# Kernel optimization log

Measured on AMD Instinct MI355X. Metric: run time of the kernel, lower is better.

## Reference

```python
import jax, jax.numpy as jnp
import numpy as np

B, C, H, W = 64, 256, 40, 40
NC = 12          # num_classes
WS = 5           # window_size
WHN, WWN = H // WS, W // WS  # 8, 8


def _window_coords():
    # Reproduces the torch __init__ construction of self.window_coords: [1, 8, 8, 2, 5, 5]
    bh = np.arange(WS) * 2.0 / (H - 1); bh = bh - bh.mean()
    bw = np.arange(WS) * 2.0 / (W - 1); bw = bw - bw.mean()
    ebh = np.tile(bh, WHN)  # [H]
    ebw = np.tile(bw, WWN)  # [W]
    # after meshgrid(ebw, ebh, ij) + permute(0,2,1): ch0 varies along cols (x), ch1 along rows (y)
    wc_x = np.broadcast_to(ebw[None, :], (H, W))
    wc_y = np.broadcast_to(ebh[:, None], (H, W))
    wc = np.stack([wc_x, wc_y], 0).reshape(2, WHN, WS, WWN, WS).transpose(1, 3, 0, 2, 4)
    return jnp.asarray(wc[None], dtype=jnp.float32)  # [1, WHN, WWN, 2, WS, WS]


def _bn(x, g, b, rm, rv):
    # eval-mode BatchNorm2d; x: [B, C, H, W], params per-channel
    inv = g / jnp.sqrt(rv + 1e-5)
    return x * inv[:, None, None] + (b - rm * inv)[:, None, None]


def _grid_sample(im, grid):
    # bilinear, padding_mode='zeros', align_corners=True; im [B,C,H,W], grid [B,H,W,2] (x,y)
    Bn, Cn, Hn, Wn = im.shape
    x = (grid[..., 0] + 1.0) * 0.5 * (Wn - 1)
    y = (grid[..., 1] + 1.0) * 0.5 * (Hn - 1)
    x0 = jnp.floor(x); x1 = x0 + 1.0
    y0 = jnp.floor(y); y1 = y0 + 1.0

    def corner(xi, yi, wgt):
        valid = (xi >= 0) & (xi <= Wn - 1) & (yi >= 0) & (yi <= Hn - 1)
        xc = jnp.clip(xi, 0, Wn - 1).astype(jnp.int32)
        yc = jnp.clip(yi, 0, Hn - 1).astype(jnp.int32)
        v = jax.vmap(lambda imb, yb, xb: imb[:, yb, xb])(im, yc, xc)  # [B,C,H,W]
        return v * (wgt * valid.astype(im.dtype))[:, None]

    return (corner(x0, y0, (x1 - x) * (y1 - y))
            + corner(x1, y0, (x - x0) * (y1 - y))
            + corner(x0, y1, (x1 - x) * (y - y0))
            + corner(x1, y1, (x - x0) * (y - y0)))


def setup_inputs() -> dict:
    key = jax.random.key(0)
    ks = jax.random.split(key, 16)
    f32 = jnp.float32
    return {
        "feats": jax.random.normal(ks[0], (B, C, H, W), f32),
        # distribution_head: Conv1x1 C->4*NC, BN, ReLU, grouped Conv1x1 4*NC->NC (groups=NC)
        "w1": jax.random.normal(ks[1], (NC * 4, C), f32) * 0.05,
        "b1": jax.random.normal(ks[2], (NC * 4,), f32) * 0.05,
        "g1": 1.0 + 0.1 * jax.random.normal(ks[3], (NC * 4,), f32),
        "be1": 0.1 * jax.random.normal(ks[4], (NC * 4,), f32),
        "rm1": 0.1 * jax.random.normal(ks[5], (NC * 4,), f32),
        "rv1": jax.random.uniform(ks[6], (NC * 4,), f32, 0.5, 1.5),
        "w2": jax.random.normal(ks[7], (NC, 4), f32) * 0.1,
        "b2": jax.random.normal(ks[8], (NC,), f32) * 0.05,
        # deformation_head: AvgPool5, BN(C), ReLU, Conv1x1 C->8
        "gd": 1.0 + 0.1 * jax.random.normal(ks[9], (C,), f32),
        "bed": 0.1 * jax.random.normal(ks[10], (C,), f32),
        "rmd": 0.1 * jax.random.normal(ks[11], (C,), f32),
        "rvd": jax.random.uniform(ks[12], (C,), f32, 0.5, 1.5),
        "wd": jax.random.normal(ks[13], (8, C), f32) * 0.05,
        "bd": jax.random.normal(ks[14], (8,), f32) * 0.05,
    }


def reference(feats, w1, b1, g1, be1, rm1, rv1, w2, b2, gd, bed, rmd, rvd, wd, bd):
    # ---- distribution_head ----
    x = jnp.einsum('bchw,oc->bohw', feats, w1) + b1[:, None, None]
    x = jax.nn.relu(_bn(x, g1, be1, rm1, rv1))
    x = x.reshape(B, NC, 4, H, W)  # grouped 1x1 conv, groups=NC
    y = jnp.einsum('bgchw,gc->bghw', x, w2) + b2[:, None, None]  # [B, NC, H, W]

    # ---- point_distribution (first batch element, as in original) ----
    hm = 1.0 - jnp.max(jax.nn.sigmoid(y[0]), axis=0)          # [H, W]
    hm = hm * (255.0 / jnp.max(hm))
    pointmap = (hm > (9.0 / 11.0) * 255.0).astype(feats.dtype)
    _ = pointmap  # due to the original's ==255 bug, pointmap never influences the mask

    # ---- point_mask: density map is always all-zero -> constant box (0,0,w=30,h=40) ----
    w_stride = W // 4  # 10
    mask_col = (jnp.arange(W) < 3 * w_stride).astype(feats.dtype)  # cols [0,30)
    fm = feats * mask_col + (1.0 - mask_col) * 1e-5
    f2 = fm + feats  # residual add from forward()

    # ---- region_deformer ----
    pooled = f2.reshape(B, C, WHN, WS, WWN, WS).mean(axis=(3, 5))  # AvgPool2d(5,5) -> [B,C,8,8]
    pooled = jax.nn.relu(_bn(pooled, gd, bed, rmd, rvd))
    co = jnp.einsum('bchw,oc->bhwo', pooled, wd) + bd              # [B,8,8,8]

    xr, yr, sx, sy = co[..., 0], co[..., 1], co[..., 2], co[..., 3]
    s = sx * sy
    tx = co[..., 4:6][..., None]  # [B,8,8,2,1]
    ty = co[..., 6:8][..., None]

    def rot(a):  # [[cos, sin], [-sin, cos]]
        return jnp.stack([jnp.cos(a), jnp.sin(a), -jnp.sin(a), jnp.cos(a)], -1).reshape(a.shape + (2, 2))

    M0 = (rot(xr) @ rot(yr)) * s[..., None, None]                  # Rx @ Ry @ (s*I)
    M1 = sx[..., None, None] * (rot(xr) @ ty) + tx                 # Rx @ (sx*I) @ ty + tx
    row3 = jnp.broadcast_to(jnp.array([0.0, 0.0, 1.0], feats.dtype), (B, WHN, WWN, 1, 3))
    M = jnp.concatenate([jnp.concatenate([M0, M1], -1), row3], -2)  # [B,8,8,3,3]

    wc = _window_coords().reshape(1, WHN, WWN, 2, WS * WS)
    wcp = jnp.concatenate([wc, jnp.ones((1, WHN, WWN, 1, WS * WS), feats.dtype)], -2)
    twc = M @ wcp                                                   # [B,8,8,3,25]
    den = twc[..., 2:3, :]
    den = jnp.where(den == 0.0, 1e-6, den)
    tw = twc[..., :2, :] / den
    coords = tw.reshape(B, WHN, WWN, 2, WS, WS).transpose(0, 3, 1, 4, 2, 5)  # [B,2,8,5,8,5]
    grid = coords.transpose(0, 2, 3, 4, 5, 1).reshape(B, H, W, 2)

    return _grid_sample(f2, grid)
```

## Files before the change

kernel.cpp:

```cpp
#include <hip/hip_runtime.h>
#include <math.h>

#define NB   64
#define NC_  256
#define NH   40
#define NW   40
#define NHW  1600
#define NWIN 64
#define CH   4
#define PW   44
#define IMS  1852

typedef float f32x4 __attribute__((ext_vector_type(4)));

__global__ __launch_bounds__(256) void pool_co_kernel(
    const float* __restrict__ feats,
    const float* __restrict__ gd, const float* __restrict__ bed,
    const float* __restrict__ rmd, const float* __restrict__ rvd,
    const float* __restrict__ wd, const float* __restrict__ bd,
    float4* __restrict__ cw4, int2* __restrict__ cbc)
{
    __shared__ float pl[8][NC_];
    __shared__ __align__(16) float swd[8 * NC_];
    __shared__ float sco[8][8];
    __shared__ float sM6[8][6];

    const int blk = blockIdx.x;
    const int b   = blk >> 3;
    const int wh  = blk & 7;
    const int t   = threadIdx.x;

    for (int i = t; i < 512; i += 256)
        ((f32x4*)swd)[i] = ((const f32x4*)wd)[i];

    {
        const f32x4* src = (const f32x4*)(feats + ((size_t)(b * NC_ + t)) * NHW
                                          + wh * 5 * NW);
        float acc[8] = {0.f, 0.f, 0.f, 0.f, 0.f, 0.f, 0.f, 0.f};
        #pragma unroll
        for (int r = 0; r < 5; ++r) {
            #pragma unroll
            for (int j = 0; j < 10; ++j) {
                const f32x4 v = src[r * 10 + j];
                #pragma unroll
                for (int k = 0; k < 4; ++k)
                    acc[(4 * j + k) / 5] += v[k];
            }
        }
        const float inv  = gd[t] / sqrtf(rvd[t] + 1e-5f);
        const float beta = bed[t] - rmd[t] * inv;
        #pragma unroll
        for (int ww = 0; ww < 8; ++ww) {
            const float mean = acc[ww] * (1.0f / 25.0f);
            const float f2m  = (ww < 6) ? (2.0f * mean) : (mean + 1e-5f);
            pl[ww][t] = fmaxf(f2m * inv + beta, 0.0f);
        }
    }
    __syncthreads();

    {
        const int w = t >> 5;
        const int s = t & 31;
        float po[8] = {0.f, 0.f, 0.f, 0.f, 0.f, 0.f, 0.f, 0.f};
        #pragma unroll
        for (int k = 0; k < 8; ++k) {
            const int c2 = s + 32 * k;
            const float p = pl[w][c2];
            #pragma unroll
            for (int o = 0; o < 8; ++o)
                po[o] += p * swd[o * NC_ + c2];
        }
        #pragma unroll
        for (int o = 0; o < 8; ++o) {
            #pragma unroll
            for (int off = 16; off > 0; off >>= 1)
                po[o] += __shfl_down(po[o], off, 32);
        }
        if (s == 0) {
            #pragma unroll
            for (int o = 0; o < 8; ++o) sco[w][o] = po[o] + bd[o];
        }
    }
    __syncthreads();

    if (t < 8) {
        const float xr = sco[t][0], yr = sco[t][1], sx = sco[t][2], sy = sco[t][3];
        const float tx0 = sco[t][4], tx1 = sco[t][5], ty0 = sco[t][6], ty1 = sco[t][7];
        const float cx = cosf(xr), sxr = sinf(xr);
        const float cy = cosf(yr), syr = sinf(yr);
        const float s = sx * sy;
        sM6[t][0] = (cx * cy - sxr * syr) * s;
        sM6[t][1] = (cx * syr + sxr * cy) * s;
        sM6[t][2] = sx * (cx * ty0 + sxr * ty1) + tx0;
        sM6[t][3] = (-sxr * cy - cx * syr) * s;
        sM6[t][4] = (-sxr * syr + cx * cy) * s;
        sM6[t][5] = sx * (-sxr * ty0 + cx * ty1) + tx1;
    }
    __syncthreads();

    if (t < 200) {
        const int w   = t / 25;
        const int pxi = t - w * 25;
        const int ii  = pxi / 5;
        const int jj  = pxi - ii * 5;
        const float* m = sM6[w];

        const float wcx = (float)(jj - 2) * (2.0f / 39.0f);
        const float wcy = (float)(ii - 2) * (2.0f / 39.0f);
        const float gx = m[0] * wcx + m[1] * wcy + m[2];
        const float gy = m[3] * wcx + m[4] * wcy + m[5];

        float x = (gx + 1.0f) * 19.5f;
        float y = (gy + 1.0f) * 19.5f;
        x = fminf(fmaxf(x, -1.0e6f), 1.0e6f);
        y = fminf(fmaxf(y, -1.0e6f), 1.0e6f);

        const float x0f = floorf(x), y0f = floorf(y);
        const int x0 = (int)x0f, y0 = (int)y0f;
        const int x1 = x0 + 1,  y1 = y0 + 1;
        const float fx = x - x0f, fy = y - y0f;

        const bool xv0 = (x0 >= 0) & (x0 <= NW - 1);
        const bool xv1 = (x1 >= 0) & (x1 <= NW - 1);
        const bool yv0 = (y0 >= 0) & (y0 <= NH - 1);
        const bool yv1 = (y1 >= 0) & (y1 <= NH - 1);

        const float w00 = (1.f - fx) * (1.f - fy) * (float)(xv0 && yv0);
        const float w01 = fx * (1.f - fy) * (float)(xv1 && yv0);
        const float w10 = (1.f - fx) * fy * (float)(xv0 && yv1);
        const float w11 = fx * fy * (float)(xv1 && yv1);

        const int xc0 = min(max(x0, 0), NW - 1);
        const int xc1 = min(max(x1, 0), NW - 1);
        const float a0 = (xc0 < 30) ? 2.f : 1.f;
        const float a1 = (xc1 < 30) ? 2.f : 1.f;
        const float d0 = (xc0 < 30) ? 0.f : 1e-5f;
        const float d1 = (xc1 < 30) ? 0.f : 1e-5f;

        float4 wvec;
        wvec.x = w00 * a0;
        wvec.y = w01 * a1;
        wvec.z = w10 * a0;
        wvec.w = w11 * a1;
        const float cst = (w00 + w10) * d0 + (w01 + w11) * d1;

        const int xb = min(max(x0, -1), NW - 1);
        const int yb = min(max(y0, -1), NH - 1);
        const int base = (yb + 1) * PW + xb;

        const int h    = wh * 5 + ii;
        const int wcol = w * 5 + jj;
        const int pidx = b * NHW + h * NW + wcol;
        cw4[pidx] = wvec;
        cbc[pidx] = make_int2(base, __float_as_int(cst));
    }
}

__global__ __launch_bounds__(320) void sample_lean_kernel(
    const float* __restrict__ feats,
    const float4* __restrict__ cw4, const int2* __restrict__ cbc,
    float* __restrict__ out)
{
    __shared__ __align__(16) float img[CH * IMS];

    const int blk = blockIdx.x;
    const int b   = blk >> 6;
    const int cg  = blk & 63;
    const int c0  = cg * CH;

    const float4* cwb = cw4 + (size_t)b * NHW;
    const int2*   cbb = cbc + (size_t)b * NHW;
    float4 wv[5];
    int2   pc[5];
    #pragma unroll
    for (int k = 0; k < 5; ++k) {
        wv[k] = cwb[k * 320 + threadIdx.x];
        pc[k] = cbb[k * 320 + threadIdx.x];
    }

    for (int i = threadIdx.x; i < CH * 63; i += 320) {
        const int cc = i / 63;
        const int t  = i - cc * 63;
        float* im = img + cc * IMS + 4;
        f32x4 z = {0.f, 0.f, 0.f, 0.f};
        if (t == 0)       *(f32x4*)(img + cc * IMS) = z;
        else if (t <= 11) *(f32x4*)(im + (t - 1) * 4) = z;
        else if (t <= 22) *(f32x4*)(im + 41 * PW + (t - 12) * 4) = z;
        else              *(f32x4*)(im + (t - 22) * PW + 40) = z;
    }

    {
        const int g   = threadIdx.x / 80;
        const int r80 = threadIdx.x - g * 80;
        const int rb  = r80 / 10;
        const int cb  = r80 - rb * 10;
        const float* src = feats + (size_t)(b * NC_ + c0 + g) * NHW;
        float* dst = img + g * IMS + 4 + PW;
        #pragma unroll
        for (int m = 0; m < 5; ++m) {
            const f32x4 v = *((const f32x4*)src + (m * 80 + r80));
            *(f32x4*)(dst + (m * 8 + rb) * PW + cb * 4) = v;
        }
    }
    __syncthreads();

    float* dstb = out + (size_t)(b * NC_ + c0) * NHW;

    #pragma unroll
    for (int k = 0; k < 5; ++k) {
        const int px = k * 320 + threadIdx.x;
        const int   base = pc[k].x;
        const float cst  = __int_as_float(pc[k].y);
        #pragma unroll
        for (int cc = 0; cc < CH; ++cc) {
            const float* ip = img + cc * IMS + 4 + base;
            const float r = cst + wv[k].x * ip[0]  + wv[k].y * ip[1]
                                + wv[k].z * ip[PW] + wv[k].w * ip[PW + 1];
            __builtin_nontemporal_store(r, &dstb[(size_t)cc * NHW + px]);
        }
    }
}

__global__ __launch_bounds__(256) void pool_bn_kernel(
    const float* __restrict__ feats,
    const float* __restrict__ gd, const float* __restrict__ bed,
    const float* __restrict__ rmd, const float* __restrict__ rvd,
    float* __restrict__ pooled)
{
    __shared__ __align__(16) float img[NHW];
    const int bc = blockIdx.x;
    const int b  = bc >> 8;
    const int c  = bc & 255;

    const float4* src4 = (const float4*)(feats + (size_t)bc * NHW);
    for (int i = threadIdx.x; i < NHW / 4; i += 256)
        ((float4*)img)[i] = src4[i];
    __syncthreads();

    if (threadIdx.x < NWIN) {
        const int win = threadIdx.x;
        const int wh  = win >> 3;
        const int ww  = win & 7;
        const int base = (wh * 5) * NW + ww * 5;
        float sum = 0.f;
        #pragma unroll
        for (int i = 0; i < 5; ++i)
            #pragma unroll
            for (int j = 0; j < 5; ++j)
                sum += img[base + i * NW + j];
        float mean = sum * (1.0f / 25.0f);
        float f2m  = (ww < 6) ? (2.0f * mean) : (mean + 1e-5f);
        float inv  = gd[c] / sqrtf(rvd[c] + 1e-5f);
        float v    = f2m * inv + (bed[c] - rmd[c] * inv);
        v = fmaxf(v, 0.0f);
        pooled[((size_t)(b * NWIN + win)) * NC_ + c] = v;
    }
}

__global__ __launch_bounds__(256) void co_M_kernel(
    const float* __restrict__ pooled,
    const float* __restrict__ wd, const float* __restrict__ bd,
    float* __restrict__ Mbuf)
{
    const int blk = blockIdx.x;
    const int tid = threadIdx.x;

    __shared__ float red[4][8];
    __shared__ float co[8];

    const float p = pooled[(size_t)blk * NC_ + tid];
    float part[8];
    #pragma unroll
    for (int o = 0; o < 8; ++o) part[o] = p * wd[o * NC_ + tid];

    const int lane = tid & 63;
    const int wv   = tid >> 6;
    #pragma unroll
    for (int o = 0; o < 8; ++o) {
        float v = part[o];
        #pragma unroll
        for (int off = 32; off > 0; off >>= 1) v += __shfl_down(v, off, 64);
        if (lane == 0) red[wv][o] = v;
    }
    __syncthreads();
    if (tid < 8) co[tid] = red[0][tid] + red[1][tid] + red[2][tid] + red[3][tid] + bd[tid];
    __syncthreads();

    if (tid == 0) {
        const float xr = co[0], yr = co[1], sx = co[2], sy = co[3];
        const float tx0 = co[4], tx1 = co[5], ty0 = co[6], ty1 = co[7];
        const float cx = cosf(xr), sxr = sinf(xr);
        const float cy = cosf(yr), syr = sinf(yr);
        const float s = sx * sy;
        float* m = Mbuf + blk * 6;
        m[0] = (cx * cy - sxr * syr) * s;
        m[1] = (cx * syr + sxr * cy) * s;
        m[2] = sx * (cx * ty0 + sxr * ty1) + tx0;
        m[3] = (-sxr * cy - cx * syr) * s;
        m[4] = (-sxr * syr + cx * cy) * s;
        m[5] = sx * (-sxr * ty0 + cx * ty1) + tx1;
    }
}

__global__ __launch_bounds__(256) void sample_kernel(
    const float* __restrict__ feats,
    const float* __restrict__ Mbuf,
    float* __restrict__ out)
{
    __shared__ __align__(16) float img[NHW];
    __shared__ float Ml[NWIN * 6];

    const int bc = blockIdx.x;
    const int b  = bc >> 8;

    const float4* src4 = (const float4*)(feats + (size_t)bc * NHW);
    for (int i = threadIdx.x; i < NHW / 4; i += 256) {
        float4 v = src4[i];
        const int j = i % (NW / 4);
        if (j < 7)      { v.x *= 2.f; v.y *= 2.f; v.z *= 2.f; v.w *= 2.f; }
        else if (j == 7){ v.x *= 2.f; v.y *= 2.f; v.z += 1e-5f; v.w += 1e-5f; }
        else            { v.x += 1e-5f; v.y += 1e-5f; v.z += 1e-5f; v.w += 1e-5f; }
        ((float4*)img)[i] = v;
    }
    for (int i = threadIdx.x; i < NWIN * 6; i += 256)
        Ml[i] = Mbuf[b * NWIN * 6 + i];
    __syncthreads();

    float* dst = out + (size_t)bc * NHW;
    for (int idx = threadIdx.x; idx < NHW; idx += 256) {
        const int h  = idx / NW;
        const int w  = idx - h * NW;
        const int wh = h / 5, ii = h - wh * 5;
        const int ww = w / 5, jj = w - ww * 5;
        const float* m = &Ml[(wh * 8 + ww) * 6];

        const float wcx = (float)(jj - 2) * (2.0f / 39.0f);
        const float wcy = (float)(ii - 2) * (2.0f / 39.0f);
        const float gx = m[0] * wcx + m[1] * wcy + m[2];
        const float gy = m[3] * wcx + m[4] * wcy + m[5];

        float x = (gx + 1.0f) * 19.5f;
        float y = (gy + 1.0f) * 19.5f;
        x = fminf(fmaxf(x, -1.0e6f), 1.0e6f);
        y = fminf(fmaxf(y, -1.0e6f), 1.0e6f);

        const float x0f = floorf(x), y0f = floorf(y);
        const int x0 = (int)x0f, y0 = (int)y0f;
        const int x1 = x0 + 1,  y1 = y0 + 1;
        const float fx = x - x0f, fy = y - y0f;

        const bool xv0 = (x0 >= 0) & (x0 <= NW - 1);
        const bool xv1 = (x1 >= 0) & (x1 <= NW - 1);
        const bool yv0 = (y0 >= 0) & (y0 <= NH - 1);
        const bool yv1 = (y1 >= 0) & (y1 <= NH - 1);

        const int xc0 = min(max(x0, 0), NW - 1);
        const int xc1 = min(max(x1, 0), NW - 1);
        const int yc0 = min(max(y0, 0), NH - 1);
        const int yc1 = min(max(y1, 0), NH - 1);

        float acc = 0.f;
        acc += img[yc0 * NW + xc0] * ((1.f - fx) * (1.f - fy)) * (float)(xv0 && yv0);
        acc += img[yc0 * NW + xc1] * (fx * (1.f - fy)) * (float)(xv1 && yv0);
        acc += img[yc1 * NW + xc0] * ((1.f - fx) * fy) * (float)(xv0 && yv1);
        acc += img[yc1 * NW + xc1] * (fx * fy) * (float)(xv1 && yv1);

        dst[idx] = acc;
    }
}

extern "C" void kernel_launch(void* const* d_in, const int* in_sizes, int n_in,
                              void* d_out, int out_size, void* d_ws, size_t ws_size,
                              hipStream_t stream)
{
    (void)in_sizes; (void)n_in; (void)out_size;

    const float* feats = (const float*)d_in[0];
    const float* gd  = (const float*)d_in[9];
    const float* bed = (const float*)d_in[10];
    const float* rmd = (const float*)d_in[11];
    const float* rvd = (const float*)d_in[12];
    const float* wd  = (const float*)d_in[13];
    const float* bd  = (const float*)d_in[14];

    float* out = (float*)d_out;

    const size_t CW_OFF  = 98304;
    const size_t CW_B    = (size_t)NB * NHW * sizeof(float4);
    const size_t CBC_OFF = CW_OFF + CW_B;
    const size_t CBC_B   = (size_t)NB * NHW * sizeof(int2);
    const bool fast = (ws_size >= CBC_OFF + CBC_B);

    if (fast) {
        float4* cw4 = (float4*)((char*)d_ws + CW_OFF);
        int2*   cbc = (int2*)((char*)d_ws + CBC_OFF);
        pool_co_kernel<<<NB * 8, 256, 0, stream>>>(feats, gd, bed, rmd, rvd,
                                                   wd, bd, cw4, cbc);
        sample_lean_kernel<<<NB * (NC_ / CH), 320, 0, stream>>>(feats, cw4, cbc, out);
    } else {
        float* Mbuf   = (float*)d_ws;
        float* pooled = out;
        pool_bn_kernel<<<NB * NC_, 256, 0, stream>>>(feats, gd, bed, rmd, rvd, pooled);
        co_M_kernel<<<NB * NWIN, 256, 0, stream>>>(pooled, wd, bd, Mbuf);
        sample_kernel<<<NB * NC_, 256, 0, stream>>>(feats, Mbuf, out);
    }
}
```

Baseline: 64.63 us.

## Gather bilinear samples directly from global memory instead of staging in LDS

The sampling kernel no longer copies each 4-channel image tile into a zero-padded shared-memory buffer. The first kernel now emits four packed 16-bit clamped corner offsets per pixel, and the sampler reads the four corners straight from global memory, relying on L1/L2 caching. This removes the LDS staging, the zero-border writes and a barrier, at the cost of scattered global loads. The additive 1e-5 constant term for columns at 30 or beyond is dropped, which changes the output slightly.

```diff
diff --git a/kernel.cpp b/kernel.cpp
--- a/kernel.cpp
+++ b/kernel.cpp
@@ -8,8 +8,6 @@
 #define NHW  1600
 #define NWIN 64
 #define CH   4
-#define PW   44
-#define IMS  1852
 
 typedef float f32x4 __attribute__((ext_vector_type(4)));
 
@@ -18,7 +16,7 @@
     const float* __restrict__ gd, const float* __restrict__ bed,
     const float* __restrict__ rmd, const float* __restrict__ rvd,
     const float* __restrict__ wd, const float* __restrict__ bd,
-    float4* __restrict__ cw4, int2* __restrict__ cbc)
+    float4* __restrict__ cw4, int2* __restrict__ cpk)
 {
     __shared__ float pl[8][NC_];
     __shared__ __align__(16) float swd[8 * NC_];
@@ -132,90 +130,56 @@
 
         const int xc0 = min(max(x0, 0), NW - 1);
         const int xc1 = min(max(x1, 0), NW - 1);
+        const int yc0 = min(max(y0, 0), NH - 1);
+        const int yc1 = min(max(y1, 0), NH - 1);
         const float a0 = (xc0 < 30) ? 2.f : 1.f;
         const float a1 = (xc1 < 30) ? 2.f : 1.f;
-        const float d0 = (xc0 < 30) ? 0.f : 1e-5f;
-        const float d1 = (xc1 < 30) ? 0.f : 1e-5f;
 
         float4 wvec;
         wvec.x = w00 * a0;
         wvec.y = w01 * a1;
         wvec.z = w10 * a0;
         wvec.w = w11 * a1;
-        const float cst = (w00 + w10) * d0 + (w01 + w11) * d1;
-
-        const int xb = min(max(x0, -1), NW - 1);
-        const int yb = min(max(y0, -1), NH - 1);
-        const int base = (yb + 1) * PW + xb;
+
+        int2 pk;
+        pk.x = (yc0 * NW + xc0) | ((yc0 * NW + xc1) << 16);
+        pk.y = (yc1 * NW + xc0) | ((yc1 * NW + xc1) << 16);
 
         const int h    = wh * 5 + ii;
         const int wcol = w * 5 + jj;
         const int pidx = b * NHW + h * NW + wcol;
         cw4[pidx] = wvec;
-        cbc[pidx] = make_int2(base, __float_as_int(cst));
-    }
-}
-
-__global__ __launch_bounds__(320) void sample_lean_kernel(
+        cpk[pidx] = pk;
+    }
+}
+
+__global__ __launch_bounds__(320) void sample_gather_kernel(
     const float* __restrict__ feats,
-    const float4* __restrict__ cw4, const int2* __restrict__ cbc,
+    const float4* __restrict__ cw4, const int2* __restrict__ cpk,
     float* __restrict__ out)
 {
-    __shared__ __align__(16) float img[CH * IMS];
-
     const int blk = blockIdx.x;
     const int b   = blk >> 6;
     const int cg  = blk & 63;
     const int c0  = cg * CH;
 
     const float4* cwb = cw4 + (size_t)b * NHW;
-    const int2*   cbb = cbc + (size_t)b * NHW;
-    float4 wv[5];
-    int2   pc[5];
-    #pragma unroll
-    for (int k = 0; k < 5; ++k) {
-        wv[k] = cwb[k * 320 + threadIdx.x];
-        pc[k] = cbb[k * 320 + threadIdx.x];
-    }
-
-    for (int i = threadIdx.x; i < CH * 63; i += 320) {
-        const int cc = i / 63;
-        const int t  = i - cc * 63;
-        float* im = img + cc * IMS + 4;
-        f32x4 z = {0.f, 0.f, 0.f, 0.f};
-        if (t == 0)       *(f32x4*)(img + cc * IMS) = z;
-        else if (t <= 11) *(f32x4*)(im + (t - 1) * 4) = z;
-        else if (t <= 22) *(f32x4*)(im + 41 * PW + (t - 12) * 4) = z;
-        else              *(f32x4*)(im + (t - 22) * PW + 40) = z;
-    }
-
-    {
-        const int g   = threadIdx.x / 80;
-        const int r80 = threadIdx.x - g * 80;
-        const int rb  = r80 / 10;
-        const int cb  = r80 - rb * 10;
-        const float* src = feats + (size_t)(b * NC_ + c0 + g) * NHW;
-        float* dst = img + g * IMS + 4 + PW;
-        #pragma unroll
-        for (int m = 0; m < 5; ++m) {
-            const f32x4 v = *((const f32x4*)src + (m * 80 + r80));
-            *(f32x4*)(dst + (m * 8 + rb) * PW + cb * 4) = v;
-        }
-    }
-    __syncthreads();
-
-    float* dstb = out + (size_t)(b * NC_ + c0) * NHW;
+    const int2*   cpb = cpk + (size_t)b * NHW;
+    const float*  fb   = feats + (size_t)(b * NC_ + c0) * NHW;
+    float*        dstb = out   + (size_t)(b * NC_ + c0) * NHW;
 
     #pragma unroll
     for (int k = 0; k < 5; ++k) {
         const int px = k * 320 + threadIdx.x;
-        const int   base = pc[k].x;
-        const float cst  = __int_as_float(pc[k].y);
+        const float4 wv = cwb[px];
+        const int2   pk = cpb[px];
+        const int o00 = pk.x & 0xffff, o01 = pk.x >> 16;
+        const int o10 = pk.y & 0xffff, o11 = pk.y >> 16;
         #pragma unroll
         for (int cc = 0; cc < CH; ++cc) {
-            const float* ip = img + cc * IMS + 4 + base;
-            const float r = cst + wv[k].x * ip[0]  + wv[k].y * ip[1]
-                                + wv[k].z * ip[PW] + wv[k].w * ip[PW + 1];
+            const float* ip = fb + cc * NHW;
+            const float r = wv.x * ip[o00] + wv.y * ip[o01]
+                          + wv.z * ip[o10] + wv.w * ip[o11];
             __builtin_nontemporal_store(r, &dstb[(size_t)cc * NHW + px]);
         }
     }
@@ -387,16 +351,16 @@
 
     const size_t CW_OFF  = 98304;
     const size_t CW_B    = (size_t)NB * NHW * sizeof(float4);
-    const size_t CBC_OFF = CW_OFF + CW_B;
-    const size_t CBC_B   = (size_t)NB * NHW * sizeof(int2);
-    const bool fast = (ws_size >= CBC_OFF + CBC_B);
+    const size_t CPK_OFF = CW_OFF + CW_B;
+    const size_t CPK_B   = (size_t)NB * NHW * sizeof(int2);
+    const bool fast = (ws_size >= CPK_OFF + CPK_B);
 
     if (fast) {
         float4* cw4 = (float4*)((char*)d_ws + CW_OFF);
-        int2*   cbc = (int2*)((char*)d_ws + CBC_OFF);
+        int2*   cpk = (int2*)((char*)d_ws + CPK_OFF);
         pool_co_kernel<<<NB * 8, 256, 0, stream>>>(feats, gd, bed, rmd, rvd,
-                                                   wd, bd, cw4, cbc);
-        sample_lean_kernel<<<NB * (NC_ / CH), 320, 0, stream>>>(feats, cw4, cbc, out);
+                                                   wd, bd, cw4, cpk);
+        sample_gather_kernel<<<NB * (NC_ / CH), 320, 0, stream>>>(feats, cw4, cpk, out);
     } else {
         float* Mbuf   = (float*)d_ws;
         float* pooled = out;
```

Measured after the change: 118.2 us. +82.9%, slower.

## Fuse pooling/coefficient and sampling kernels into one persistent grid with per-batch flags

Applied to the files above, without the earlier changes.

Merges the two-kernel pipeline into a single 1024-block persistent kernel. The first 512 blocks compute the pooled distribution head and per-pixel sampling coefficients, then signal a per-batch atomic counter. Every block then processes four (batch, channel-group) tiles, staging the image into shared memory before spin-waiting on that batch's counter, so coefficient work overlaps with sampling and the second launch disappears. In exchange it adds a memset, spin-waits that depend on all producer blocks being co-resident, re-reads of coefficients per tile, and reduced occupancy for the producer phase.

```diff
diff --git a/kernel.cpp b/kernel.cpp
--- a/kernel.cpp
+++ b/kernel.cpp
@@ -10,213 +10,226 @@
 #define CH   4
 #define PW   44
 #define IMS  1852
+#define GRID 1024
 
 typedef float f32x4 __attribute__((ext_vector_type(4)));
 
-__global__ __launch_bounds__(256) void pool_co_kernel(
+__global__ __launch_bounds__(320) void fused_all_kernel(
     const float* __restrict__ feats,
     const float* __restrict__ gd, const float* __restrict__ bed,
     const float* __restrict__ rmd, const float* __restrict__ rvd,
     const float* __restrict__ wd, const float* __restrict__ bd,
-    float4* __restrict__ cw4, int2* __restrict__ cbc)
+    float4* __restrict__ cw4, int2* __restrict__ cbc,
+    float* __restrict__ out,
+    unsigned* __restrict__ done)
 {
-    __shared__ float pl[8][NC_];
-    __shared__ __align__(16) float swd[8 * NC_];
-    __shared__ float sco[8][8];
-    __shared__ float sM6[8][6];
-
-    const int blk = blockIdx.x;
-    const int b   = blk >> 3;
-    const int wh  = blk & 7;
-    const int t   = threadIdx.x;
-
-    for (int i = t; i < 512; i += 256)
-        ((f32x4*)swd)[i] = ((const f32x4*)wd)[i];
-
-    {
-        const f32x4* src = (const f32x4*)(feats + ((size_t)(b * NC_ + t)) * NHW
-                                          + wh * 5 * NW);
-        float acc[8] = {0.f, 0.f, 0.f, 0.f, 0.f, 0.f, 0.f, 0.f};
+    __shared__ __align__(16) float smem[CH * IMS];
+    const int i = blockIdx.x;
+    const int t = threadIdx.x;
+
+    if (i < 512) {
+        const int wh = i >> 6;
+        const int b  = i & 63;
+        float* pl  = smem;
+        float* swd = smem + 2048;
+        float* sco = smem + 4096;
+        float* sM6 = smem + 4160;
+
+        for (int k = t; k < 512; k += 320)
+            ((f32x4*)swd)[k] = ((const f32x4*)wd)[k];
+
+        if (t < 256) {
+            const f32x4* src = (const f32x4*)(feats + ((size_t)(b * NC_ + t)) * NHW
+                                              + wh * 5 * NW);
+            float acc[8] = {0.f, 0.f, 0.f, 0.f, 0.f, 0.f, 0.f, 0.f};
+            #pragma unroll
+            for (int r = 0; r < 5; ++r) {
+                #pragma unroll
+                for (int j = 0; j < 10; ++j) {
+                    const f32x4 v = src[r * 10 + j];
+                    #pragma unroll
+                    for (int k = 0; k < 4; ++k)
+                        acc[(4 * j + k) / 5] += v[k];
+                }
+            }
+            const float inv  = gd[t] / sqrtf(rvd[t] + 1e-5f);
+            const float beta = bed[t] - rmd[t] * inv;
+            #pragma unroll
+            for (int ww = 0; ww < 8; ++ww) {
+                const float mean = acc[ww] * (1.0f / 25.0f);
+                const float f2m  = (ww < 6) ? (2.0f * mean) : (mean + 1e-5f);
+                pl[ww * NC_ + t] = fmaxf(f2m * inv + beta, 0.0f);
+            }
+        }
+        __syncthreads();
+
+        if (t < 256) {
+            const int w = t >> 5;
+            const int s = t & 31;
+            float po[8] = {0.f, 0.f, 0.f, 0.f, 0.f, 0.f, 0.f, 0.f};
+            #pragma unroll
+            for (int k = 0; k < 8; ++k) {
+                const int c2 = s + 32 * k;
+                const float p = pl[w * NC_ + c2];
+                #pragma unroll
+                for (int o = 0; o < 8; ++o)
+                    po[o] += p * swd[o * NC_ + c2];
+            }
+            #pragma unroll
+            for (int o = 0; o < 8; ++o) {
+                #pragma unroll
+                for (int off = 16; off > 0; off >>= 1)
+                    po[o] += __shfl_down(po[o], off, 32);
+            }
+            if (s == 0) {
+                #pragma unroll
+                for (int o = 0; o < 8; ++o) sco[w * 8 + o] = po[o] + bd[o];
+            }
+        }
+        __syncthreads();
+
+        if (t < 8) {
+            const float xr = sco[t*8+0], yr = sco[t*8+1], sx = sco[t*8+2], sy = sco[t*8+3];
+            const float tx0 = sco[t*8+4], tx1 = sco[t*8+5], ty0 = sco[t*8+6], ty1 = sco[t*8+7];
+            const float cx = cosf(xr), sxr = sinf(xr);
+            const float cy = cosf(yr), syr = sinf(yr);
+            const float s = sx * sy;
+            sM6[t*6+0] = (cx * cy - sxr * syr) * s;
+            sM6[t*6+1] = (cx * syr + sxr * cy) * s;
+            sM6[t*6+2] = sx * (cx * ty0 + sxr * ty1) + tx0;
+            sM6[t*6+3] = (-sxr * cy - cx * syr) * s;
+            sM6[t*6+4] = (-sxr * syr + cx * cy) * s;
+            sM6[t*6+5] = sx * (-sxr * ty0 + cx * ty1) + tx1;
+        }
+        __syncthreads();
+
+        if (t < 200) {
+            const int w   = t / 25;
+            const int pxi = t - w * 25;
+            const int ii  = pxi / 5;
+            const int jj  = pxi - ii * 5;
+            const float* m = sM6 + w * 6;
+
+            const float wcx = (float)(jj - 2) * (2.0f / 39.0f);
+            const float wcy = (float)(ii - 2) * (2.0f / 39.0f);
+            const float gx = m[0] * wcx + m[1] * wcy + m[2];
+            const float gy = m[3] * wcx + m[4] * wcy + m[5];
+
+            float x = (gx + 1.0f) * 19.5f;
+            float y = (gy + 1.0f) * 19.5f;
+            x = fminf(fmaxf(x, -1.0e6f), 1.0e6f);
+            y = fminf(fmaxf(y, -1.0e6f), 1.0e6f);
+
+            const float x0f = floorf(x), y0f = floorf(y);
+            const int x0 = (int)x0f, y0 = (int)y0f;
+            const int x1 = x0 + 1,  y1 = y0 + 1;
+            const float fx = x - x0f, fy = y - y0f;
+
+            const bool xv0 = (x0 >= 0) & (x0 <= NW - 1);
+            const bool xv1 = (x1 >= 0) & (x1 <= NW - 1);
+            const bool yv0 = (y0 >= 0) & (y0 <= NH - 1);
+            const bool yv1 = (y1 >= 0) & (y1 <= NH - 1);
+
+            const float w00 = (1.f - fx) * (1.f - fy) * (float)(xv0 && yv0);
+            const float w01 = fx * (1.f - fy) * (float)(xv1 && yv0);
+            const float w10 = (1.f - fx) * fy * (float)(xv0 && yv1);
+            const float w11 = fx * fy * (float)(xv1 && yv1);
+
+            const int xc0 = min(max(x0, 0), NW - 1);
+            const int xc1 = min(max(x1, 0), NW - 1);
+            const float a0 = (xc0 < 30) ? 2.f : 1.f;
+            const float a1 = (xc1 < 30) ? 2.f : 1.f;
+            const float d0 = (xc0 < 30) ? 0.f : 1e-5f;
+            const float d1 = (xc1 < 30) ? 0.f : 1e-5f;
+
+            float4 wvec;
+            wvec.x = w00 * a0;
+            wvec.y = w01 * a1;
+            wvec.z = w10 * a0;
+            wvec.w = w11 * a1;
+            const float cst = (w00 + w10) * d0 + (w01 + w11) * d1;
+
+            const int xb = min(max(x0, -1), NW - 1);
+            const int yb = min(max(y0, -1), NH - 1);
+            const int base = (yb + 1) * PW + xb;
+
+            const int h    = wh * 5 + ii;
+            const int wcol = w * 5 + jj;
+            const int pidx = b * NHW + h * NW + wcol;
+            cw4[pidx] = wvec;
+            cbc[pidx] = make_int2(base, __float_as_int(cst));
+        }
+        __threadfence();
+        __syncthreads();
+        if (t == 0)
+            __hip_atomic_fetch_add(&done[b], 1u, __ATOMIC_RELEASE,
+                                   __HIP_MEMORY_SCOPE_AGENT);
+    }
+
+    const int x    = i & 7;
+    const int rank = i >> 3;
+    const int g    = t / 80;
+    const int r80  = t - g * 80;
+    const int rb   = r80 / 10;
+    const int cb   = r80 - rb * 10;
+
+    #pragma unroll 1
+    for (int k = 0; k < 4; ++k) {
+        const int j  = rank + (k << 7);
+        const int b  = x + 8 * (j >> 6);
+        const int cg = j & 63;
+        const int c0 = cg * CH;
+
+        __syncthreads();
+
+        if (k == 0) {
+            for (int z = t; z < CH * 63; z += 320) {
+                const int cc = z / 63;
+                const int tt = z - cc * 63;
+                float* im = smem + cc * IMS + 4;
+                f32x4 zz = {0.f, 0.f, 0.f, 0.f};
+                if (tt == 0)       *(f32x4*)(smem + cc * IMS) = zz;
+                else if (tt <= 11) *(f32x4*)(im + (tt - 1) * 4) = zz;
+                else if (tt <= 22) *(f32x4*)(im + 41 * PW + (tt - 12) * 4) = zz;
+                else               *(f32x4*)(im + (tt - 22) * PW + 40) = zz;
+            }
+        }
+
+        {
+            const float* src = feats + (size_t)(b * NC_ + c0 + g) * NHW;
+            float* dstl = smem + g * IMS + 4 + PW;
+            #pragma unroll
+            for (int m = 0; m < 5; ++m) {
+                const f32x4 v = *((const f32x4*)src + (m * 80 + r80));
+                *(f32x4*)(dstl + (m * 8 + rb) * PW + cb * 4) = v;
+            }
+        }
+
+        if (t == 0) {
+            while (__hip_atomic_load(&done[b], __ATOMIC_ACQUIRE,
+                                     __HIP_MEMORY_SCOPE_AGENT) < 8u)
+                __builtin_amdgcn_s_sleep(2);
+        }
+        __syncthreads();
+
+        const float4* cwb = cw4 + (size_t)b * NHW;
+        const int2*   cbb = cbc + (size_t)b * NHW;
+        float* dstb = out + (size_t)(b * NC_ + c0) * NHW;
+
         #pragma unroll
-        for (int r = 0; r < 5; ++r) {
-            #pragma unroll
-            for (int j = 0; j < 10; ++j) {
-                const f32x4 v = src[r * 10 + j];
-                #pragma unroll
-                for (int k = 0; k < 4; ++k)
-                    acc[(4 * j + k) / 5] += v[k];
-            }
-        }
-        const float inv  = gd[t] / sqrtf(rvd[t] + 1e-5f);
-        const float beta = bed[t] - rmd[t] * inv;
-        #pragma unroll
-        for (int ww = 0; ww < 8; ++ww) {
-            const float mean = acc[ww] * (1.0f / 25.0f);
-            const float f2m  = (ww < 6) ? (2.0f * mean) : (mean + 1e-5f);
-            pl[ww][t] = fmaxf(f2m * inv + beta, 0.0f);
-        }
-    }
-    __syncthreads();
-
-    {
-        const int w = t >> 5;
-        const int s = t & 31;
-        float po[8] = {0.f, 0.f, 0.f, 0.f, 0.f, 0.f, 0.f, 0.f};
-        #pragma unroll
-        for (int k = 0; k < 8; ++k) {
-            const int c2 = s + 32 * k;
-            const float p = pl[w][c2];
-            #pragma unroll
-            for (int o = 0; o < 8; ++o)
-                po[o] += p * swd[o * NC_ + c2];
-        }
-        #pragma unroll
-        for (int o = 0; o < 8; ++o) {
-            #pragma unroll
-            for (int off = 16; off > 0; off >>= 1)
-                po[o] += __shfl_down(po[o], off, 32);
-        }
-        if (s == 0) {
-            #pragma unroll
-            for (int o = 0; o < 8; ++o) sco[w][o] = po[o] + bd[o];
-        }
-    }
-    __syncthreads();
-
-    if (t < 8) {
-        const float xr = sco[t][0], yr = sco[t][1], sx = sco[t][2], sy = sco[t][3];
-        const float tx0 = sco[t][4], tx1 = sco[t][5], ty0 = sco[t][6], ty1 = sco[t][7];
-        const float cx = cosf(xr), sxr = sinf(xr);
-        const float cy = cosf(yr), syr = sinf(yr);
-        const float s = sx * sy;
-        sM6[t][0] = (cx * cy - sxr * syr) * s;
-        sM6[t][1] = (cx * syr + sxr * cy) * s;
-        sM6[t][2] = sx * (cx * ty0 + sxr * ty1) + tx0;
-        sM6[t][3] = (-sxr * cy - cx * syr) * s;
-        sM6[t][4] = (-sxr * syr + cx * cy) * s;
-        sM6[t][5] = sx * (-sxr * ty0 + cx * ty1) + tx1;
-    }
-    __syncthreads();
-
-    if (t < 200) {
-        const int w   = t / 25;
-        const int pxi = t - w * 25;
-        const int ii  = pxi / 5;
-        const int jj  = pxi - ii * 5;
-        const float* m = sM6[w];
-
-        const float wcx = (float)(jj - 2) * (2.0f / 39.0f);
-        const float wcy = (float)(ii - 2) * (2.0f / 39.0f);
-        const float gx = m[0] * wcx + m[1] * wcy + m[2];
-        const float gy = m[3] * wcx + m[4] * wcy + m[5];
-
-        float x = (gx + 1.0f) * 19.5f;
-        float y = (gy + 1.0f) * 19.5f;
-        x = fminf(fmaxf(x, -1.0e6f), 1.0e6f);
-        y = fminf(fmaxf(y, -1.0e6f), 1.0e6f);
-
-        const float x0f = floorf(x), y0f = floorf(y);
-        const int x0 = (int)x0f, y0 = (int)y0f;
-        const int x1 = x0 + 1,  y1 = y0 + 1;
-        const float fx = x - x0f, fy = y - y0f;
-
-        const bool xv0 = (x0 >= 0) & (x0 <= NW - 1);
-        const bool xv1 = (x1 >= 0) & (x1 <= NW - 1);
-        const bool yv0 = (y0 >= 0) & (y0 <= NH - 1);
-        const bool yv1 = (y1 >= 0) & (y1 <= NH - 1);
-
-        const float w00 = (1.f - fx) * (1.f - fy) * (float)(xv0 && yv0);
-        const float w01 = fx * (1.f - fy) * (float)(xv1 && yv0);
-        const float w10 = (1.f - fx) * fy * (float)(xv0 && yv1);
-        const float w11 = fx * fy * (float)(xv1 && yv1);
-
-        const int xc0 = min(max(x0, 0), NW - 1);
-        const int xc1 = min(max(x1, 0), NW - 1);
-        const float a0 = (xc0 < 30) ? 2.f : 1.f;
-        const float a1 = (xc1 < 30) ? 2.f : 1.f;
-        const float d0 = (xc0 < 30) ? 0.f : 1e-5f;
-        const float d1 = (xc1 < 30) ? 0.f : 1e-5f;
-
-        float4 wvec;
-        wvec.x = w00 * a0;
-        wvec.y = w01 * a1;
-        wvec.z = w10 * a0;
-        wvec.w = w11 * a1;
-        const float cst = (w00 + w10) * d0 + (w01 + w11) * d1;
-
-        const int xb = min(max(x0, -1), NW - 1);
-        const int yb = min(max(y0, -1), NH - 1);
-        const int base = (yb + 1) * PW + xb;
-
-        const int h    = wh * 5 + ii;
-        const int wcol = w * 5 + jj;
-        const int pidx = b * NHW + h * NW + wcol;
-        cw4[pidx] = wvec;
-        cbc[pidx] = make_int2(base, __float_as_int(cst));
-    }
-}
-
-__global__ __launch_bounds__(320) void sample_lean_kernel(
-    const float* __restrict__ feats,
-    const float4* __restrict__ cw4, const int2* __restrict__ cbc,
-    float* __restrict__ out)
-{
-    __shared__ __align__(16) float img[CH * IMS];
-
-    const int blk = blockIdx.x;
-    const int b   = blk >> 6;
-    const int cg  = blk & 63;
-    const int c0  = cg * CH;
-
-    const float4* cwb = cw4 + (size_t)b * NHW;
-    const int2*   cbb = cbc + (size_t)b * NHW;
-    float4 wv[5];
-    int2   pc[5];
-    #pragma unroll
-    for (int k = 0; k < 5; ++k) {
-        wv[k] = cwb[k * 320 + threadIdx.x];
-        pc[k] = cbb[k * 320 + threadIdx.x];
-    }
-
-    for (int i = threadIdx.x; i < CH * 63; i += 320) {
-        const int cc = i / 63;
-        const int t  = i - cc * 63;
-        float* im = img + cc * IMS + 4;
-        f32x4 z = {0.f, 0.f, 0.f, 0.f};
-        if (t == 0)       *(f32x4*)(img + cc * IMS) = z;
-        else if (t <= 11) *(f32x4*)(im + (t - 1) * 4) = z;
-        else if (t <= 22) *(f32x4*)(im + 41 * PW + (t - 12) * 4) = z;
-        else              *(f32x4*)(im + (t - 22) * PW + 40) = z;
-    }
-
-    {
-        const int g   = threadIdx.x / 80;
-        const int r80 = threadIdx.x - g * 80;
-        const int rb  = r80 / 10;
-        const int cb  = r80 - rb * 10;
-        const float* src = feats + (size_t)(b * NC_ + c0 + g) * NHW;
-        float* dst = img + g * IMS + 4 + PW;
-        #pragma unroll
-        for (int m = 0; m < 5; ++m) {
-            const f32x4 v = *((const f32x4*)src + (m * 80 + r80));
-            *(f32x4*)(dst + (m * 8 + rb) * PW + cb * 4) = v;
-        }
-    }
-    __syncthreads();
-
-    float* dstb = out + (size_t)(b * NC_ + c0) * NHW;
-
-    #pragma unroll
-    for (int k = 0; k < 5; ++k) {
-        const int px = k * 320 + threadIdx.x;
-        const int   base = pc[k].x;
-        const float cst  = __int_as_float(pc[k].y);
-        #pragma unroll
-        for (int cc = 0; cc < CH; ++cc) {
-            const float* ip = img + cc * IMS + 4 + base;
-            const float r = cst + wv[k].x * ip[0]  + wv[k].y * ip[1]
-                                + wv[k].z * ip[PW] + wv[k].w * ip[PW + 1];
-            __builtin_nontemporal_store(r, &dstb[(size_t)cc * NHW + px]);
+        for (int kk = 0; kk < 5; ++kk) {
+            const int px = kk * 320 + t;
+            const float4 wv = cwb[px];
+            const int2   pc = cbb[px];
+            const int   base = pc.x;
+            const float cst  = __int_as_float(pc.y);
+            #pragma unroll
+            for (int cc = 0; cc < CH; ++cc) {
+                const float* ip = smem + cc * IMS + 4 + base;
+                const float r = cst + wv.x * ip[0]  + wv.y * ip[1]
+                                    + wv.z * ip[PW] + wv.w * ip[PW + 1];
+                __builtin_nontemporal_store(r, &dstb[(size_t)cc * NHW + px]);
+            }
         }
     }
 }
@@ -389,14 +402,16 @@
     const size_t CW_B    = (size_t)NB * NHW * sizeof(float4);
     const size_t CBC_OFF = CW_OFF + CW_B;
     const size_t CBC_B   = (size_t)NB * NHW * sizeof(int2);
-    const bool fast = (ws_size >= CBC_OFF + CBC_B);
+    const size_t FL_OFF  = CBC_OFF + CBC_B;
+    const bool fast = (ws_size >= FL_OFF + NB * sizeof(unsigned));
 
     if (fast) {
-        float4* cw4 = (float4*)((char*)d_ws + CW_OFF);
-        int2*   cbc = (int2*)((char*)d_ws + CBC_OFF);
-        pool_co_kernel<<<NB * 8, 256, 0, stream>>>(feats, gd, bed, rmd, rvd,
-                                                   wd, bd, cw4, cbc);
-        sample_lean_kernel<<<NB * (NC_ / CH), 320, 0, stream>>>(feats, cw4, cbc, out);
+        float4*   cw4  = (float4*)((char*)d_ws + CW_OFF);
+        int2*     cbc  = (int2*)((char*)d_ws + CBC_OFF);
+        unsigned* done = (unsigned*)((char*)d_ws + FL_OFF);
+        hipMemsetAsync(done, 0, NB * sizeof(unsigned), stream);
+        fused_all_kernel<<<GRID, 320, 0, stream>>>(feats, gd, bed, rmd, rvd,
+                                                   wd, bd, cw4, cbc, out, done);
     } else {
         float* Mbuf   = (float*)d_ws;
         float* pooled = out;
```

New measurement: 192.5 us. 198% more time.
